# Kernel optimization log

Hardware: AMD Instinct MI355X
Metric: run time of the kernel (lower is better)

## Reference

```python
import jax, jax.numpy as jnp
import numpy as np

N = 50000
E = 800000
NFEAT, NHID, NCLASS = 128, 64, 16


def _spmm(row, col, w, x):
    # out[i] = sum_{e: row[e]==i} w[e] * x[col[e]]  -- sparse adj @ x
    return jax.ops.segment_sum(x[col] * w[:, None], row, num_segments=N)


def _gcn_layer(x, row, col, w, W, b):
    return _spmm(row, col, w, x @ W) + b


def setup_inputs() -> dict:
    key = jax.random.key(0)
    ks = jax.random.split(key, 16)
    glorot = lambda k, fi, fo: jax.random.uniform(k, (fi, fo), jnp.float32, -1.0, 1.0) / jnp.sqrt(fi)
    inp = {
        "x": jax.random.normal(ks[0], (N, NFEAT), jnp.float32),
        "edge_row": jax.random.randint(ks[1], (E,), 0, N, jnp.int32),
        "edge_col": jax.random.randint(ks[2], (E,), 0, N, jnp.int32),
        "edge_weight": jax.random.uniform(ks[3], (E,), jnp.float32),
        "W1": glorot(ks[4], NFEAT, NHID), "b1": jnp.zeros((NHID,), jnp.float32),
        "W2": glorot(ks[5], NHID, NHID), "b2": jnp.zeros((NHID,), jnp.float32),
        "W3": glorot(ks[6], NHID, NHID), "b3": jnp.zeros((NHID,), jnp.float32),
        "W4": glorot(ks[7], NHID, NHID), "b4": jnp.zeros((NHID,), jnp.float32),
        "W5": glorot(ks[8], NHID, NCLASS), "b5": jnp.zeros((NCLASS,), jnp.float32),
    }
    return inp


def reference(x, edge_row, edge_col, edge_weight, W1, b1, W2, b2, W3, b3, W4, b4, W5, b5):
    # Inference mode: dropout is identity.
    e1 = _gcn_layer(x, edge_row, edge_col, edge_weight, W1, b1)
    h = jax.nn.relu(e1)
    e2 = _gcn_layer(h, edge_row, edge_col, edge_weight, W2, b2)
    h = jax.nn.relu(e2)
    e3 = _gcn_layer(h, edge_row, edge_col, edge_weight, W3, b3)
    h = jax.nn.relu(e3)
    e4 = _gcn_layer(h, edge_row, edge_col, edge_weight, W4, b4)
    h = jax.nn.relu(e4)
    e5 = _gcn_layer(h, edge_row, edge_col, edge_weight, W5, b5)
    return (jax.nn.log_softmax(e5, axis=1), e1, e2, e3, e4, e5)
```

## Files before the change

kernel.cpp:

```cpp
#include <hip/hip_runtime.h>
#include <math.h>

#define NN 50000
#define NE 800000
#define NFEAT 128
#define NHID 64
#define NCLASS 16
#define NB_SCAN ((NN + 255) / 256)
#define GB ((NN + 63) / 64)
#define SGRP 4
#define ROWS_PER_SGRP ((NN + SGRP - 1) / SGRP)
#define SCHUNKS 392
#define EMAX 1024

__device__ inline unsigned short f2bf(float f) {
    unsigned u = __builtin_bit_cast(unsigned, f);
    u += 0x7fffu + ((u >> 16) & 1u);
    return (unsigned short)(u >> 16);
}
__device__ inline float bf2f(unsigned short h) {
    return __builtin_bit_cast(float, (unsigned)h << 16);
}
__device__ inline float pk_w(unsigned v) { return bf2f((unsigned short)(v >> 16)); }
__device__ inline int pk_c(unsigned v) { return (int)(v & 0xffffu); }


__global__ __launch_bounds__(256) void hist_pack_kernel(const int* __restrict__ erow,
                                                        const int* __restrict__ ecol,
                                                        const float* __restrict__ ew,
                                                        int* __restrict__ deg,
                                                        uint2* __restrict__ rr8, int E) {
    int e = blockIdx.x * 256 + threadIdx.x;
    if (e < E) {
        int r = erow[e];
        int k = atomicAdd(&deg[r], 1);
        uint2 v;
        v.x = ((unsigned)r << 16) | (unsigned)k;
        v.y = ((unsigned)f2bf(ew[e]) << 16) | (unsigned)ecol[e];
        rr8[e] = v;
    }
}

__global__ __launch_bounds__(256) void scan_sum_kernel(const int* __restrict__ deg,
                                                       int* __restrict__ blocksum, int n) {
    __shared__ int s[256];
    const int t = threadIdx.x;
    int i = blockIdx.x * 256 + t;
    s[t] = (i < n) ? deg[i] : 0;
    __syncthreads();
#pragma unroll
    for (int off = 128; off > 0; off >>= 1) {
        if (t < off) s[t] += s[t + off];
        __syncthreads();
    }
    if (t == 0) blocksum[blockIdx.x] = s[0];
}

__global__ __launch_bounds__(256) void scan_final_kernel(const int* __restrict__ deg,
                                                         const int* __restrict__ blocksum,
                                                         int* __restrict__ row_ptr, int n) {
    __shared__ int bs[256];
    __shared__ int s[256];
    const int t = threadIdx.x;
    bs[t] = (t < NB_SCAN) ? blocksum[t] : 0;
    __syncthreads();
    for (int off = 1; off < 256; off <<= 1) {
        int u = (t >= off) ? bs[t - off] : 0;
        __syncthreads();
        bs[t] += u;
        __syncthreads();
    }
    const int blockpre = (blockIdx.x == 0) ? 0 : bs[blockIdx.x - 1];

    int i = blockIdx.x * 256 + t;
    int d = (i < n) ? deg[i] : 0;
    s[t] = d;
    __syncthreads();
    for (int off = 1; off < 256; off <<= 1) {
        int u = (t >= off) ? s[t - off] : 0;
        __syncthreads();
        s[t] += u;
        __syncthreads();
    }
    int excl = blockpre + s[t] - d;
    if (i < n) {
        row_ptr[i] = excl;
        if (i == n - 1) row_ptr[n] = excl + d;
    }
}

__global__ __launch_bounds__(256) void scatter_rank8_kernel(const uint2* __restrict__ rr8,
                                                            const int* __restrict__ row_ptr,
                                                            unsigned* __restrict__ pk, int E) {
    const int g = blockIdx.x & (SGRP - 1);
    const int chunk = blockIdx.x / SGRP;
    const int CH = (E + SCHUNKS - 1) / SCHUNKS;
    const int lo = chunk * CH;
    const int hi = (lo + CH < E) ? lo + CH : E;
    const int rlo = g * ROWS_PER_SGRP;
    const int rhi = (rlo + ROWS_PER_SGRP < NN) ? rlo + ROWS_PER_SGRP : NN;
    for (int e = lo + threadIdx.x; e < hi; e += 256) {
        uint2 v = rr8[e];
        int r = (int)(v.x >> 16);
        if (r >= rlo && r < rhi) {
            pk[row_ptr[r] + (int)(v.x & 0xffffu)] = v.y;
        }
    }
}

template <int K, bool RELU_IN>
__global__ __launch_bounds__(256) void gemm64_kernel(const float* __restrict__ in,
                                                     const float* __restrict__ Wg,
                                                     unsigned short* __restrict__ outb, int M) {
    constexpr int KC = 64;
    __shared__ float xs[KC][68];
    __shared__ float Ws[KC][64];
    const int t = threadIdx.x;
    const int tx = t % 16;
    const int ty = t / 16;
    const int r0 = blockIdx.x * 64;

    float acc[4][4];
#pragma unroll
    for (int i = 0; i < 4; i++)
#pragma unroll
        for (int j = 0; j < 4; j++) acc[i][j] = 0.f;

    for (int k0 = 0; k0 < K; k0 += KC) {
        for (int i = t * 4; i < KC * 64; i += 1024) {
            *(float4*)&Ws[i / 64][i % 64] = *(const float4*)&Wg[(size_t)k0 * 64 + i];
        }
        {
            const int r = t / 4;
            const int q = t % 4;
            const int gr = r0 + r;
#pragma unroll
            for (int i = 0; i < 4; i++) {
                int k = q * 16 + i * 4;
                float4 v;
                if (gr < M)
                    v = *(const float4*)&in[(size_t)gr * K + k0 + k];
                else
                    v = make_float4(0.f, 0.f, 0.f, 0.f);
                if (RELU_IN) {
                    v.x = fmaxf(v.x, 0.f);
                    v.y = fmaxf(v.y, 0.f);
                    v.z = fmaxf(v.z, 0.f);
                    v.w = fmaxf(v.w, 0.f);
                }
                xs[k + 0][r] = v.x;
                xs[k + 1][r] = v.y;
                xs[k + 2][r] = v.z;
                xs[k + 3][r] = v.w;
            }
        }
        __syncthreads();
#pragma unroll 8
        for (int k = 0; k < KC; k++) {
            float4 xv = *(const float4*)&xs[k][ty * 4];
            float4 wv = *(const float4*)&Ws[k][tx * 4];
            acc[0][0] += xv.x * wv.x; acc[0][1] += xv.x * wv.y;
            acc[0][2] += xv.x * wv.z; acc[0][3] += xv.x * wv.w;
            acc[1][0] += xv.y * wv.x; acc[1][1] += xv.y * wv.y;
            acc[1][2] += xv.y * wv.z; acc[1][3] += xv.y * wv.w;
            acc[2][0] += xv.z * wv.x; acc[2][1] += xv.z * wv.y;
            acc[2][2] += xv.z * wv.z; acc[2][3] += xv.z * wv.w;
            acc[3][0] += xv.w * wv.x; acc[3][1] += xv.w * wv.y;
            acc[3][2] += xv.w * wv.z; acc[3][3] += xv.w * wv.w;
        }
        __syncthreads();
    }
#pragma unroll
    for (int i = 0; i < 4; i++) {
        int r = r0 + ty * 4 + i;
        if (r < M) {
            ushort4 u;
            u.x = f2bf(acc[i][0]);
            u.y = f2bf(acc[i][1]);
            u.z = f2bf(acc[i][2]);
            u.w = f2bf(acc[i][3]);
            *(ushort4*)&outb[(size_t)r * 64 + tx * 4] = u;
        }
    }
}

template <int NOUT>
__global__ __launch_bounds__(256, 8) void spmm64_fused_kernel(
    const unsigned short* __restrict__ gb,
    const int* __restrict__ row_ptr,
    const unsigned* __restrict__ pk,
    const float* __restrict__ bias,
    const float* __restrict__ Wn,
    float* __restrict__ e_out,
    unsigned short* __restrict__ nxt,
    int M) {
    __shared__ float xs[8][64];
    __shared__ unsigned epk[EMAX];
    const int t = threadIdx.x;
    const int lane = t & 63;
    const int rb = t >> 5;
    const int slot = (lane >> 4) & 1;
    const int fl = (lane & 15) * 4;

    const int blk0 = blockIdx.x * 8;
    const int base = row_ptr[blk0];
    const int cnt = row_ptr[blk0 + 8] - base;
    const bool fits = (cnt <= EMAX);
    if (fits) {
        for (int i = t; i < cnt; i += 256) epk[i] = pk[base + i];
    }
    __syncthreads();

    const int r = blk0 + rb;
    float a0 = 0.f, a1 = 0.f, a2 = 0.f, a3 = 0.f;

#define FMA_EDGE(q, g)                                              \
    {                                                               \
        float w_ = pk_w(q);                                         \
        a0 += w_ * bf2f((unsigned short)((g).x & 0xffffu));         \
        a1 += w_ * bf2f((unsigned short)((g).x >> 16));             \
        a2 += w_ * bf2f((unsigned short)((g).y & 0xffffu));         \
        a3 += w_ * bf2f((unsigned short)((g).y >> 16));             \
    }
#define GLD(q) (*(const uint2*)&gb[(size_t)pk_c(q) * 64 + fl])

    if (fits) {
        int le = row_ptr[r] - base;
        const int lend = row_ptr[r + 1] - base;
        for (; le + 16 <= lend; le += 16) {
            unsigned q0 = epk[le + 0 + slot], q1 = epk[le + 2 + slot];
            unsigned q2 = epk[le + 4 + slot], q3 = epk[le + 6 + slot];
            unsigned q4 = epk[le + 8 + slot], q5 = epk[le + 10 + slot];
            unsigned q6 = epk[le + 12 + slot], q7 = epk[le + 14 + slot];
            uint2 g0 = GLD(q0), g1 = GLD(q1), g2 = GLD(q2), g3 = GLD(q3);
            uint2 g4 = GLD(q4), g5 = GLD(q5), g6 = GLD(q6), g7 = GLD(q7);
            FMA_EDGE(q0, g0); FMA_EDGE(q1, g1); FMA_EDGE(q2, g2); FMA_EDGE(q3, g3);
            FMA_EDGE(q4, g4); FMA_EDGE(q5, g5); FMA_EDGE(q6, g6); FMA_EDGE(q7, g7);
        }
        if (le + 8 <= lend) {
            unsigned q0 = epk[le + 0 + slot], q1 = epk[le + 2 + slot];
            unsigned q2 = epk[le + 4 + slot], q3 = epk[le + 6 + slot];
            uint2 g0 = GLD(q0), g1 = GLD(q1), g2 = GLD(q2), g3 = GLD(q3);
            FMA_EDGE(q0, g0); FMA_EDGE(q1, g1); FMA_EDGE(q2, g2); FMA_EDGE(q3, g3);
            le += 8;
        }
        if (le + 4 <= lend) {
            unsigned q0 = epk[le + 0 + slot], q1 = epk[le + 2 + slot];
            uint2 g0 = GLD(q0), g1 = GLD(q1);
            FMA_EDGE(q0, g0); FMA_EDGE(q1, g1);
            le += 4;
        }
        if (le + 2 <= lend) {
            unsigned q = epk[le + slot];
            uint2 g = GLD(q);
            FMA_EDGE(q, g);
            le += 2;
        }
        if (le < lend && slot == 0) {
            unsigned q = epk[le];
            uint2 g = GLD(q);
            FMA_EDGE(q, g);
        }
    } else {
        int e = row_ptr[r];
        const int end = row_ptr[r + 1];
        for (; e + 2 <= end; e += 2) {
            unsigned q = pk[e + slot];
            uint2 g = GLD(q);
            FMA_EDGE(q, g);
        }
        if (e < end && slot == 0) {
            unsigned q = pk[e];
            uint2 g = GLD(q);
            FMA_EDGE(q, g);
        }
    }
#undef FMA_EDGE
#undef GLD

    a0 += __shfl_xor(a0, 16);
    a1 += __shfl_xor(a1, 16);
    a2 += __shfl_xor(a2, 16);
    a3 += __shfl_xor(a3, 16);

    if (slot == 0) {
        float4 b4 = *(const float4*)&bias[fl];
        float4 v;
        v.x = a0 + b4.x;
        v.y = a1 + b4.y;
        v.z = a2 + b4.z;
        v.w = a3 + b4.w;
        *(float4*)&e_out[(size_t)r * 64 + fl] = v;
        xs[rb][fl + 0] = fmaxf(v.x, 0.f);
        xs[rb][fl + 1] = fmaxf(v.y, 0.f);
        xs[rb][fl + 2] = fmaxf(v.z, 0.f);
        xs[rb][fl + 3] = fmaxf(v.w, 0.f);
    }
    __syncthreads();

    if (NOUT == 64) {
        const int rblk = t >> 6;
        const int j = t & 63;
        float acc0 = 0.f, acc1 = 0.f;
#pragma unroll 16
        for (int k = 0; k < 64; k++) {
            float w = Wn[k * 64 + j];
            acc0 += xs[rblk][k] * w;
            acc1 += xs[rblk + 4][k] * w;
        }
        nxt[(size_t)(blk0 + rblk) * 64 + j] = f2bf(acc0);
        nxt[(size_t)(blk0 + rblk + 4) * 64 + j] = f2bf(acc1);
    } else {
        if (t < 8 * NOUT) {
            const int rr = t / NOUT;
            const int j = t % NOUT;
            float acc = 0.f;
#pragma unroll 16
            for (int k = 0; k < 64; k++) acc += xs[rr][k] * Wn[k * NOUT + j];
            nxt[(size_t)(blk0 + rr) * NOUT + j] = f2bf(acc);
        }
    }
}

__global__ __launch_bounds__(256) void spmm16_lsm_kernel(const unsigned short* __restrict__ tmpc,
                                                         const int* __restrict__ row_ptr,
                                                         const unsigned* __restrict__ pk,
                                                         const float* __restrict__ bias,
                                                         float* __restrict__ e5,
                                                         float* __restrict__ out0, int M) {
    const int t = threadIdx.x;
    const int wv = __builtin_amdgcn_readfirstlane(t >> 6);
    const int lane = t & 63;
    const int f = lane & 15;
    const int s = lane >> 4;
    const int r = blockIdx.x * 4 + wv;
    if (r >= M) return;

    int e = row_ptr[r];
    const int end = row_ptr[r + 1];
    float acc = 0.f;
    for (; e + 8 <= end; e += 8) {
        unsigned qa = pk[e + s];
        unsigned qb = pk[e + 4 + s];
        acc += pk_w(qa) * bf2f(tmpc[(size_t)pk_c(qa) * 16 + f]);
        acc += pk_w(qb) * bf2f(tmpc[(size_t)pk_c(qb) * 16 + f]);
    }
    if (e + 4 <= end) {
        unsigned q = pk[e + s];
        acc += pk_w(q) * bf2f(tmpc[(size_t)pk_c(q) * 16 + f]);
        e += 4;
    }
    if (s < end - e) {
        unsigned q = pk[e + s];
        acc += pk_w(q) * bf2f(tmpc[(size_t)pk_c(q) * 16 + f]);
    }
    acc += __shfl_xor(acc, 16);
    acc += __shfl_xor(acc, 32);
    float v = acc + bias[f];

    float m = v;
#pragma unroll
    for (int off = 1; off < 16; off <<= 1) m = fmaxf(m, __shfl_xor(m, off, 16));
    float sum = expf(v - m);
#pragma unroll
    for (int off = 1; off < 16; off <<= 1) sum += __shfl_xor(sum, off, 16);
    float ls = logf(sum);
    if (lane < 16) {
        e5[(size_t)r * 16 + f] = v;
        out0[(size_t)r * 16 + f] = v - m - ls;
    }
}


extern "C" void kernel_launch(void* const* d_in, const int* in_sizes, int n_in,
                              void* d_out, int out_size, void* d_ws, size_t ws_size,
                              hipStream_t stream) {
    const float* x = (const float*)d_in[0];
    const int* erow = (const int*)d_in[1];
    const int* ecol = (const int*)d_in[2];
    const float* ew = (const float*)d_in[3];
    const float* W1 = (const float*)d_in[4];
    const float* b1 = (const float*)d_in[5];
    const float* W2 = (const float*)d_in[6];
    const float* b2 = (const float*)d_in[7];
    const float* W3 = (const float*)d_in[8];
    const float* b3 = (const float*)d_in[9];
    const float* W4 = (const float*)d_in[10];
    const float* b4 = (const float*)d_in[11];
    const float* W5 = (const float*)d_in[12];
    const float* b5 = (const float*)d_in[13];

    float* out0 = (float*)d_out;
    float* e1 = out0 + (size_t)NN * NCLASS;
    float* e2 = e1 + (size_t)NN * NHID;
    float* e3 = e2 + (size_t)NN * NHID;
    float* e4 = e3 + (size_t)NN * NHID;
    float* e5 = e4 + (size_t)NN * NHID;

    char* ws = (char*)d_ws;
    unsigned short* tmpA = (unsigned short*)ws; ws += (size_t)NN * NHID * 2;
    unsigned short* tmpB = (unsigned short*)ws; ws += (size_t)NN * NHID * 2;
    unsigned short* tmpc = (unsigned short*)ws; ws += ((size_t)NN * NCLASS * 2 + 255) / 256 * 256;
    int* deg = (int*)ws;      ws += ((size_t)NN * 4 + 255) / 256 * 256;
    int* row_ptr = (int*)ws;  ws += ((size_t)(NN + 1) * 4 + 255) / 256 * 256;
    int* blocksum = (int*)ws; ws += ((size_t)NB_SCAN * 4 + 255) / 256 * 256;
    uint2* rr8 = (uint2*)ws;  ws += (size_t)NE * 8;
    unsigned* pk = (unsigned*)ws; ws += (size_t)NE * 4;

    hipMemsetAsync(deg, 0, (size_t)NN * 4, stream);
    hist_pack_kernel<<<(NE + 255) / 256, 256, 0, stream>>>(erow, ecol, ew, deg, rr8, NE);
    scan_sum_kernel<<<NB_SCAN, 256, 0, stream>>>(deg, blocksum, NN);
    scan_final_kernel<<<NB_SCAN, 256, 0, stream>>>(deg, blocksum, row_ptr, NN);
    scatter_rank8_kernel<<<SGRP * SCHUNKS, 256, 0, stream>>>(rr8, row_ptr, pk, NE);

    gemm64_kernel<NFEAT, false><<<GB, 256, 0, stream>>>(x, W1, tmpA, NN);

    const int FG = NN / 8;
    spmm64_fused_kernel<64><<<FG, 256, 0, stream>>>(tmpA, row_ptr, pk, b1, W2, e1, tmpB, NN);
    spmm64_fused_kernel<64><<<FG, 256, 0, stream>>>(tmpB, row_ptr, pk, b2, W3, e2, tmpA, NN);
    spmm64_fused_kernel<64><<<FG, 256, 0, stream>>>(tmpA, row_ptr, pk, b3, W4, e3, tmpB, NN);
    spmm64_fused_kernel<16><<<FG, 256, 0, stream>>>(tmpB, row_ptr, pk, b4, W5, e4, tmpc, NN);

    spmm16_lsm_kernel<<<(NN + 3) / 4, 256, 0, stream>>>(tmpc, row_ptr, pk, b5, e5, out0, NN);
}
```

Before: 306.3 us.

## Fuse histogram with first GEMM, merge scan kernels, restage final SpMM edges

The edge histogram/pack pass and the first dense x@W1 GEMM now run in one launch, with even blocks doing the GEMM and odd blocks doing the histogram. The two-pass scan becomes a single kernel in which each block recomputes its own prefix by summing all earlier degrees. The final 16-wide SpMM with log-softmax now stages edges in LDS and gives each lane 4 features and 16 edges per pass. These cut launch count and overlap independent work, but the new GEMM is a simpler 8-row tile that reads W1 from global memory, and the merged scan does redundant quadratic prefix reads.

```diff
diff --git a/kernel.cpp b/kernel.cpp
--- a/kernel.cpp
+++ b/kernel.cpp
@@ -7,11 +7,13 @@
 #define NHID 64
 #define NCLASS 16
 #define NB_SCAN ((NN + 255) / 256)
-#define GB ((NN + 63) / 64)
 #define SGRP 4
 #define ROWS_PER_SGRP ((NN + SGRP - 1) / SGRP)
 #define SCHUNKS 392
 #define EMAX 1024
+#define EMAX4 512
+#define NTILE8 (NN / 8)
+#define HG_GEMM 2048
 
 __device__ inline unsigned short f2bf(float f) {
     unsigned u = __builtin_bit_cast(unsigned, f);
@@ -24,55 +26,65 @@
 __device__ inline float pk_w(unsigned v) { return bf2f((unsigned short)(v >> 16)); }
 __device__ inline int pk_c(unsigned v) { return (int)(v & 0xffffu); }
 
-
-__global__ __launch_bounds__(256) void hist_pack_kernel(const int* __restrict__ erow,
-                                                        const int* __restrict__ ecol,
-                                                        const float* __restrict__ ew,
-                                                        int* __restrict__ deg,
-                                                        uint2* __restrict__ rr8, int E) {
-    int e = blockIdx.x * 256 + threadIdx.x;
-    if (e < E) {
-        int r = erow[e];
-        int k = atomicAdd(&deg[r], 1);
-        uint2 v;
-        v.x = ((unsigned)r << 16) | (unsigned)k;
-        v.y = ((unsigned)f2bf(ew[e]) << 16) | (unsigned)ecol[e];
-        rr8[e] = v;
-    }
-}
-
-__global__ __launch_bounds__(256) void scan_sum_kernel(const int* __restrict__ deg,
-                                                       int* __restrict__ blocksum, int n) {
+__global__ __launch_bounds__(256) void hist_gemm_kernel(
+    const float* __restrict__ x, const float* __restrict__ W1,
+    unsigned short* __restrict__ tmpA,
+    const int* __restrict__ erow, const int* __restrict__ ecol,
+    const float* __restrict__ ew, int* __restrict__ deg,
+    uint2* __restrict__ rr8) {
+    __shared__ float xg[8 * 128];
+    const int t = threadIdx.x;
+    if ((blockIdx.x & 1) == 0) {
+        const int j = t & 63;
+        const int half = t >> 6;
+        const int lr = t >> 5;
+        const int lc = (t & 31) * 4;
+        for (int tile = blockIdx.x >> 1; tile < NTILE8; tile += HG_GEMM) {
+            const int r0 = tile * 8;
+            *(float4*)&xg[lr * 128 + lc] = *(const float4*)&x[(size_t)(r0 + lr) * 128 + lc];
+            __syncthreads();
+            float acc0 = 0.f, acc1 = 0.f;
+#pragma unroll 8
+            for (int k = 0; k < 128; k++) {
+                float w = W1[k * 64 + j];
+                acc0 += xg[half * 128 + k] * w;
+                acc1 += xg[(half + 4) * 128 + k] * w;
+            }
+            tmpA[(size_t)(r0 + half) * 64 + j] = f2bf(acc0);
+            tmpA[(size_t)(r0 + half + 4) * 64 + j] = f2bf(acc1);
+            __syncthreads();
+        }
+    } else {
+        for (int e = (blockIdx.x >> 1) * 256 + t; e < NE; e += HG_GEMM * 256) {
+            int r = erow[e];
+            int k = atomicAdd(&deg[r], 1);
+            uint2 v;
+            v.x = ((unsigned)r << 16) | (unsigned)k;
+            v.y = ((unsigned)f2bf(ew[e]) << 16) | (unsigned)ecol[e];
+            rr8[e] = v;
+        }
+    }
+}
+
+__global__ __launch_bounds__(256) void scan_merged_kernel(const int* __restrict__ deg,
+                                                          int* __restrict__ row_ptr, int n) {
     __shared__ int s[256];
     const int t = threadIdx.x;
-    int i = blockIdx.x * 256 + t;
-    s[t] = (i < n) ? deg[i] : 0;
+    const int c = blockIdx.x;
+
+    int part = 0;
+    for (int i = t; i < c * 256; i += 256) part += deg[i];
+    s[t] = part;
     __syncthreads();
 #pragma unroll
     for (int off = 128; off > 0; off >>= 1) {
         if (t < off) s[t] += s[t + off];
         __syncthreads();
     }
-    if (t == 0) blocksum[blockIdx.x] = s[0];
-}
-
-__global__ __launch_bounds__(256) void scan_final_kernel(const int* __restrict__ deg,
-                                                         const int* __restrict__ blocksum,
-                                                         int* __restrict__ row_ptr, int n) {
-    __shared__ int bs[256];
-    __shared__ int s[256];
-    const int t = threadIdx.x;
-    bs[t] = (t < NB_SCAN) ? blocksum[t] : 0;
-    __syncthreads();
-    for (int off = 1; off < 256; off <<= 1) {
-        int u = (t >= off) ? bs[t - off] : 0;
-        __syncthreads();
-        bs[t] += u;
-        __syncthreads();
-    }
-    const int blockpre = (blockIdx.x == 0) ? 0 : bs[blockIdx.x - 1];
-
-    int i = blockIdx.x * 256 + t;
+    const int blockpre = s[0];
+    __syncthreads();
+
+    int i = c * 256 + t;
     int d = (i < n) ? deg[i] : 0;
     s[t] = d;
     __syncthreads();
@@ -104,82 +116,6 @@
         int r = (int)(v.x >> 16);
         if (r >= rlo && r < rhi) {
             pk[row_ptr[r] + (int)(v.x & 0xffffu)] = v.y;
-        }
-    }
-}
-
-template <int K, bool RELU_IN>
-__global__ __launch_bounds__(256) void gemm64_kernel(const float* __restrict__ in,
-                                                     const float* __restrict__ Wg,
-                                                     unsigned short* __restrict__ outb, int M) {
-    constexpr int KC = 64;
-    __shared__ float xs[KC][68];
-    __shared__ float Ws[KC][64];
-    const int t = threadIdx.x;
-    const int tx = t % 16;
-    const int ty = t / 16;
-    const int r0 = blockIdx.x * 64;
-
-    float acc[4][4];
-#pragma unroll
-    for (int i = 0; i < 4; i++)
-#pragma unroll
-        for (int j = 0; j < 4; j++) acc[i][j] = 0.f;
-
-    for (int k0 = 0; k0 < K; k0 += KC) {
-        for (int i = t * 4; i < KC * 64; i += 1024) {
-            *(float4*)&Ws[i / 64][i % 64] = *(const float4*)&Wg[(size_t)k0 * 64 + i];
-        }
-        {
-            const int r = t / 4;
-            const int q = t % 4;
-            const int gr = r0 + r;
-#pragma unroll
-            for (int i = 0; i < 4; i++) {
-                int k = q * 16 + i * 4;
-                float4 v;
-                if (gr < M)
-                    v = *(const float4*)&in[(size_t)gr * K + k0 + k];
-                else
-                    v = make_float4(0.f, 0.f, 0.f, 0.f);
-                if (RELU_IN) {
-                    v.x = fmaxf(v.x, 0.f);
-                    v.y = fmaxf(v.y, 0.f);
-                    v.z = fmaxf(v.z, 0.f);
-                    v.w = fmaxf(v.w, 0.f);
-                }
-                xs[k + 0][r] = v.x;
-                xs[k + 1][r] = v.y;
-                xs[k + 2][r] = v.z;
-                xs[k + 3][r] = v.w;
-            }
-        }
-        __syncthreads();
-#pragma unroll 8
-        for (int k = 0; k < KC; k++) {
-            float4 xv = *(const float4*)&xs[k][ty * 4];
-            float4 wv = *(const float4*)&Ws[k][tx * 4];
-            acc[0][0] += xv.x * wv.x; acc[0][1] += xv.x * wv.y;
-            acc[0][2] += xv.x * wv.z; acc[0][3] += xv.x * wv.w;
-            acc[1][0] += xv.y * wv.x; acc[1][1] += xv.y * wv.y;
-            acc[1][2] += xv.y * wv.z; acc[1][3] += xv.y * wv.w;
-            acc[2][0] += xv.z * wv.x; acc[2][1] += xv.z * wv.y;
-            acc[2][2] += xv.z * wv.z; acc[2][3] += xv.z * wv.w;
-            acc[3][0] += xv.w * wv.x; acc[3][1] += xv.w * wv.y;
-            acc[3][2] += xv.w * wv.z; acc[3][3] += xv.w * wv.w;
-        }
-        __syncthreads();
-    }
-#pragma unroll
-    for (int i = 0; i < 4; i++) {
-        int r = r0 + ty * 4 + i;
-        if (r < M) {
-            ushort4 u;
-            u.x = f2bf(acc[i][0]);
-            u.y = f2bf(acc[i][1]);
-            u.z = f2bf(acc[i][2]);
-            u.w = f2bf(acc[i][3]);
-            *(ushort4*)&outb[(size_t)r * 64 + tx * 4] = u;
         }
     }
 }
@@ -275,7 +211,6 @@
             FMA_EDGE(q, g);
         }
     }
-#undef FMA_EDGE
 #undef GLD
 
     a0 += __shfl_xor(a0, 16);
@@ -322,52 +257,92 @@
     }
 }
 
-__global__ __launch_bounds__(256) void spmm16_lsm_kernel(const unsigned short* __restrict__ tmpc,
-                                                         const int* __restrict__ row_ptr,
-                                                         const unsigned* __restrict__ pk,
-                                                         const float* __restrict__ bias,
-                                                         float* __restrict__ e5,
-                                                         float* __restrict__ out0, int M) {
+__global__ __launch_bounds__(256, 8) void spmm16_lsm_kernel(const unsigned short* __restrict__ tmpc,
+                                                            const int* __restrict__ row_ptr,
+                                                            const unsigned* __restrict__ pk,
+                                                            const float* __restrict__ bias,
+                                                            float* __restrict__ e5,
+                                                            float* __restrict__ out0, int M) {
+    __shared__ unsigned epk[EMAX4];
     const int t = threadIdx.x;
-    const int wv = __builtin_amdgcn_readfirstlane(t >> 6);
     const int lane = t & 63;
-    const int f = lane & 15;
-    const int s = lane >> 4;
-    const int r = blockIdx.x * 4 + wv;
-    if (r >= M) return;
-
-    int e = row_ptr[r];
-    const int end = row_ptr[r + 1];
-    float acc = 0.f;
-    for (; e + 8 <= end; e += 8) {
-        unsigned qa = pk[e + s];
-        unsigned qb = pk[e + 4 + s];
-        acc += pk_w(qa) * bf2f(tmpc[(size_t)pk_c(qa) * 16 + f]);
-        acc += pk_w(qb) * bf2f(tmpc[(size_t)pk_c(qb) * 16 + f]);
-    }
-    if (e + 4 <= end) {
-        unsigned q = pk[e + s];
-        acc += pk_w(q) * bf2f(tmpc[(size_t)pk_c(q) * 16 + f]);
-        e += 4;
-    }
-    if (s < end - e) {
-        unsigned q = pk[e + s];
-        acc += pk_w(q) * bf2f(tmpc[(size_t)pk_c(q) * 16 + f]);
-    }
-    acc += __shfl_xor(acc, 16);
-    acc += __shfl_xor(acc, 32);
-    float v = acc + bias[f];
-
-    float m = v;
+    const int wv = t >> 6;
+    const int sl = lane >> 2;
+    const int fq = (lane & 3) * 4;
+
+    const int blk0 = blockIdx.x * 4;
+    const int base = row_ptr[blk0];
+    const int cnt = row_ptr[blk0 + 4] - base;
+    const bool fits = (cnt <= EMAX4);
+    if (fits) {
+        for (int i = t; i < cnt; i += 256) epk[i] = pk[base + i];
+    }
+    __syncthreads();
+
+    const int r = blk0 + wv;
+    float a0 = 0.f, a1 = 0.f, a2 = 0.f, a3 = 0.f;
+#define FMA_EDGE(q, g)                                      \
+    {                                                       \
+        float w_ = pk_w(q);                                 \
+        a0 += w_ * bf2f((unsigned short)((g).x & 0xffffu)); \
+        a1 += w_ * bf2f((unsigned short)((g).x >> 16));     \
+        a2 += w_ * bf2f((unsigned short)((g).y & 0xffffu)); \
+        a3 += w_ * bf2f((unsigned short)((g).y >> 16));     \
+    }
+#define GLD16(q) (*(const uint2*)&tmpc[(size_t)pk_c(q) * 16 + fq])
+    if (fits) {
+        int le = row_ptr[r] - base;
+        const int lend = row_ptr[r + 1] - base;
+        for (; le + 16 <= lend; le += 16) {
+            unsigned q = epk[le + sl];
+            uint2 g = GLD16(q);
+            FMA_EDGE(q, g);
+        }
+        int rem = lend - le;
+        if (sl < rem) {
+            unsigned q = epk[le + sl];
+            uint2 g = GLD16(q);
+            FMA_EDGE(q, g);
+        }
+    } else {
+        int e = row_ptr[r];
+        const int e1 = row_ptr[r + 1];
+        for (; e + 16 <= e1; e += 16) {
+            unsigned q = pk[e + sl];
+            uint2 g = GLD16(q);
+            FMA_EDGE(q, g);
+        }
+        int rem = e1 - e;
+        if (sl < rem) {
+            unsigned q = pk[e + sl];
+            uint2 g = GLD16(q);
+            FMA_EDGE(q, g);
+        }
+    }
+#undef GLD16
+#undef FMA_EDGE
 #pragma unroll
-    for (int off = 1; off < 16; off <<= 1) m = fmaxf(m, __shfl_xor(m, off, 16));
-    float sum = expf(v - m);
-#pragma unroll
-    for (int off = 1; off < 16; off <<= 1) sum += __shfl_xor(sum, off, 16);
-    float ls = logf(sum);
-    if (lane < 16) {
-        e5[(size_t)r * 16 + f] = v;
-        out0[(size_t)r * 16 + f] = v - m - ls;
+    for (int off = 4; off < 64; off <<= 1) {
+        a0 += __shfl_xor(a0, off);
+        a1 += __shfl_xor(a1, off);
+        a2 += __shfl_xor(a2, off);
+        a3 += __shfl_xor(a3, off);
+    }
+    float4 b4 = *(const float4*)&bias[fq];
+    float v0 = a0 + b4.x, v1 = a1 + b4.y, v2 = a2 + b4.z, v3 = a3 + b4.w;
+
+    float m = fmaxf(fmaxf(v0, v1), fmaxf(v2, v3));
+    m = fmaxf(m, __shfl_xor(m, 1));
+    m = fmaxf(m, __shfl_xor(m, 2));
+    float s = expf(v0 - m) + expf(v1 - m) + expf(v2 - m) + expf(v3 - m);
+    s += __shfl_xor(s, 1);
+    s += __shfl_xor(s, 2);
+    float ls = logf(s) + m;
+    if (lane < 4) {
+        float4 ev = make_float4(v0, v1, v2, v3);
+        *(float4*)&e5[(size_t)r * 16 + fq] = ev;
+        float4 ov = make_float4(v0 - ls, v1 - ls, v2 - ls, v3 - ls);
+        *(float4*)&out0[(size_t)r * 16 + fq] = ov;
     }
 }
 
@@ -403,17 +378,16 @@
     unsigned short* tmpc = (unsigned short*)ws; ws += ((size_t)NN * NCLASS * 2 + 255) / 256 * 256;
     int* deg = (int*)ws;      ws += ((size_t)NN * 4 + 255) / 256 * 256;
     int* row_ptr = (int*)ws;  ws += ((size_t)(NN + 1) * 4 + 255) / 256 * 256;
-    int* blocksum = (int*)ws; ws += ((size_t)NB_SCAN * 4 + 255) / 256 * 256;
     uint2* rr8 = (uint2*)ws;  ws += (size_t)NE * 8;
     unsigned* pk = (unsigned*)ws; ws += (size_t)NE * 4;
 
     hipMemsetAsync(deg, 0, (size_t)NN * 4, stream);
-    hist_pack_kernel<<<(NE + 255) / 256, 256, 0, stream>>>(erow, ecol, ew, deg, rr8, NE);
-    scan_sum_kernel<<<NB_SCAN, 256, 0, stream>>>(deg, blocksum, NN);
-    scan_final_kernel<<<NB_SCAN, 256, 0, stream>>>(deg, blocksum, row_ptr, NN);
+
+    hist_gemm_kernel<<<2 * HG_GEMM, 256, 0, stream>>>(x, W1, tmpA, erow, ecol, ew, deg, rr8);
+
+    scan_merged_kernel<<<NB_SCAN, 256, 0, stream>>>(deg, row_ptr, NN);
+
     scatter_rank8_kernel<<<SGRP * SCHUNKS, 256, 0, stream>>>(rr8, row_ptr, pk, NE);
-
-    gemm64_kernel<NFEAT, false><<<GB, 256, 0, stream>>>(x, W1, tmpA, NN);
 
     const int FG = NN / 8;
     spmm64_fused_kernel<64><<<FG, 256, 0, stream>>>(tmpA, row_ptr, pk, b1, W2, e1, tmpB, NN);
```

Measured after the change: 330.4 us. 7.9% more time.
